# Performance work log

Measured on AMD Instinct MI355X. Metric: run time of the kernel, lower is better.

Reference implementation:

```python
import jax, jax.numpy as jnp
import numpy as np

D_MODEL = 1024  # scaling uses sqrt(d_model), as in the source


def setup_inputs() -> dict:
    key = jax.random.key(0)
    kx, kq, kk, kv = jax.random.split(key, 4)
    B, N, D, H = 4, 4096, D_MODEL, 128
    X = jax.random.normal(kx, (B, N, D), dtype=jnp.float32)
    # nn.Linear(d_model, d_head, bias=False) weights, stored as [d_model, d_head]
    s = 1.0 / np.sqrt(D)
    Wq = jax.random.normal(kq, (D, H), dtype=jnp.float32) * s
    Wk = jax.random.normal(kk, (D, H), dtype=jnp.float32) * s
    Wv = jax.random.normal(kv, (D, H), dtype=jnp.float32) * s
    return {"X": X, "Wq": Wq, "Wk": Wk, "Wv": Wv}


def reference(X, Wq, Wk, Wv):
    # Q, K, V: [B, N, H]
    Q = jnp.einsum("bnd,dh->bnh", X, Wq)
    K = jnp.einsum("bnd,dh->bnh", X, Wk)
    V = jnp.einsum("bnd,dh->bnh", X, Wv)
    # Scores: [B, N, N]; source divides by sqrt(d_model) (not sqrt(d_head))
    A = jnp.einsum("bqh,bkh->bqk", Q, K) / jnp.sqrt(jnp.float32(D_MODEL))
    A = jax.nn.softmax(A, axis=-1)
    # Dropout is identity in eval mode (deterministic reference baseline)
    return jnp.einsum("bqk,bkh->bqh", A, V)
```

## Files before the change

kernel.cpp:

```cpp
#include <hip/hip_runtime.h>
#include <stdint.h>

typedef __bf16 bf16_t;
typedef bf16_t bf16x8 __attribute__((ext_vector_type(8)));
typedef float f32x4 __attribute__((ext_vector_type(4)));
typedef float f32x16 __attribute__((ext_vector_type(16)));
typedef unsigned short u16;
typedef unsigned int u32;

#define MFMA16(a, b, c) __builtin_amdgcn_mfma_f32_16x16x32_bf16((a), (b), (c), 0, 0, 0)
#define MFMA32(a, b, c) __builtin_amdgcn_mfma_f32_32x32x16_bf16((a), (b), (c), 0, 0, 0)

#define QSCALE 0.04508422002778633f

__device__ __forceinline__ u16 f2bf(float f) {
  union { float f; unsigned u; } v; v.f = f;
  unsigned r = v.u + 0x7fffu + ((v.u >> 16) & 1u);
  return (u16)(r >> 16);
}

__device__ __forceinline__ float exp2x(float x) {
#if __has_builtin(__builtin_amdgcn_exp2f)
  return __builtin_amdgcn_exp2f(x);
#else
  return exp2f(x);
#endif
}

__device__ __forceinline__ float rcpx(float x) {
#if __has_builtin(__builtin_amdgcn_rcpf)
  return __builtin_amdgcn_rcpf(x);
#else
  return 1.0f / x;
#endif
}

__device__ __forceinline__ void async_cp16(const void* g, void* l) {
  __builtin_amdgcn_global_load_lds(
      (__attribute__((address_space(1))) void*)(void*)g,
      (__attribute__((address_space(3))) void*)l, 16, 0, 0);
}

__device__ __forceinline__ u32 cvtpk(float lo, float hi) {
  u32 r;
  asm("v_cvt_pk_bf16_f32 %0, %1, %2" : "=v"(r) : "v"(lo), "v"(hi));
  return r;
}
__device__ __forceinline__ void pl32swap(u32& a, u32& b) {
  asm volatile("v_permlane32_swap_b32 %0, %1" : "+v"(a), "+v"(b));
}

__global__ __launch_bounds__(256) void pack_w_k(const float* __restrict__ Wq,
                                                const float* __restrict__ Wk,
                                                const float* __restrict__ Wv,
                                                u16* __restrict__ wp) {
  int t = blockIdx.x * 256 + threadIdx.x;
  int mat = t >> 14;
  int rr = t & 16383;
  int frag = rr >> 6, lane = rr & 63;
  int nt = frag >> 5, kc = frag & 31;
  const float* W = (mat == 0) ? Wq : ((mat == 1) ? Wk : Wv);
  int k0 = kc * 32 + ((lane >> 4) << 3);
  int col = nt * 16 + (lane & 15);
  union { u16 h[8]; uint4 q; } u_;
#pragma unroll
  for (int j = 0; j < 8; ++j) u_.h[j] = f2bf(W[(size_t)(k0 + j) * 128 + col]);
  *(uint4*)(wp + (size_t)t * 8) = u_.q;
}

__global__ __launch_bounds__(256) void qkv_k(const float* __restrict__ X,
                                             const u16* __restrict__ wp,
                                             u16* __restrict__ Qb,
                                             u16* __restrict__ Kb,
                                             u16* __restrict__ Vt) {
  __shared__ __align__(16) char xs[2][4096];
  const int tid = threadIdx.x;
  const int w = tid >> 6, lane = tid & 63;
  const int r16 = lane >> 4, c16 = lane & 15;
  const int m0 = blockIdx.x * 32;

  f32x4 acc[2][6];
#pragma unroll
  for (int mt = 0; mt < 2; ++mt)
#pragma unroll
    for (int i = 0; i < 6; ++i) acc[mt][i] = (f32x4){0.f, 0.f, 0.f, 0.f};

  const int srow = tid >> 3, scol = tid & 7;
  const float* sbase = X + (size_t)(m0 + srow) * 1024 + scol * 8;
  const int soff = srow * 128 + ((scol * 16) ^ ((srow & 7) << 4));

  {
    float4 v0 = *(const float4*)(sbase);
    float4 v1 = *(const float4*)(sbase + 4);
    union { u16 h[8]; uint4 q; } u_;
    u_.h[0] = f2bf(v0.x); u_.h[1] = f2bf(v0.y); u_.h[2] = f2bf(v0.z); u_.h[3] = f2bf(v0.w);
    u_.h[4] = f2bf(v1.x); u_.h[5] = f2bf(v1.y); u_.h[6] = f2bf(v1.z); u_.h[7] = f2bf(v1.w);
    *(uint4*)(xs[0] + soff) = u_.q;
  }
  __syncthreads();

  for (int kc = 0; kc < 16; ++kc) {
    float4 n0, n1;
    const bool pfch = (kc + 1) < 16;
    if (pfch) {
      n0 = *(const float4*)(sbase + (kc + 1) * 64);
      n1 = *(const float4*)(sbase + (kc + 1) * 64 + 4);
    }
    const char* xb = xs[kc & 1];
    bf16x8 a[2][2];
#pragma unroll
    for (int mt = 0; mt < 2; ++mt)
#pragma unroll
      for (int ks = 0; ks < 2; ++ks) {
        int row = mt * 16 + c16;
        int off = row * 128 + (((ks * 64) + r16 * 16) ^ ((row & 7) << 4));
        a[mt][ks] = *(const bf16x8*)(xb + off);
      }
#pragma unroll
    for (int i = 0; i < 6; ++i) {
      int t = w + 4 * i;
      int mat = t >> 3, nt = t & 7;
      const u16* bp = wp + (size_t)mat * 131072 +
                      (size_t)((nt * 32 + kc * 2) * 64 + lane) * 8;
#pragma unroll
      for (int ks = 0; ks < 2; ++ks) {
        bf16x8 b = *(const bf16x8*)(bp + (size_t)ks * 512);
#pragma unroll
        for (int mt = 0; mt < 2; ++mt) acc[mt][i] = MFMA16(a[mt][ks], b, acc[mt][i]);
      }
    }
    if (pfch) {
      union { u16 h[8]; uint4 q; } u_;
      u_.h[0] = f2bf(n0.x); u_.h[1] = f2bf(n0.y); u_.h[2] = f2bf(n0.z); u_.h[3] = f2bf(n0.w);
      u_.h[4] = f2bf(n1.x); u_.h[5] = f2bf(n1.y); u_.h[6] = f2bf(n1.z); u_.h[7] = f2bf(n1.w);
      *(uint4*)(xs[(kc + 1) & 1] + soff) = u_.q;
    }
    __syncthreads();
  }

  const int batch = m0 >> 12;
#pragma unroll
  for (int i = 0; i < 6; ++i) {
    int t = w + 4 * i;
    int mat = t >> 3, nt = t & 7;
#pragma unroll
    for (int mt = 0; mt < 2; ++mt) {
      f32x4 v = acc[mt][i];
      if (mat == 2) {
        int d = nt * 16 + c16;
        int nloc = (m0 & 4095) + mt * 16 + r16 * 4;
        union { u16 h[4]; uint2 q; } u_;
#pragma unroll
        for (int r = 0; r < 4; ++r) u_.h[r] = f2bf(v[r]);
        *(uint2*)(Vt + ((size_t)(batch * 128 + d)) * 4096 + nloc) = u_.q;
      } else {
        u16* dstm = (mat == 0) ? Qb : Kb;
        float sc = (mat == 0) ? QSCALE : 1.0f;
#pragma unroll
        for (int r = 0; r < 4; ++r) {
          int row = m0 + mt * 16 + r16 * 4 + r;
          dstm[(size_t)row * 128 + nt * 16 + c16] = f2bf(v[r] * sc);
        }
      }
    }
  }
}

__global__ __launch_bounds__(256) void pack_kv_k(const u16* __restrict__ Kb,
                                                 const u16* __restrict__ Vt,
                                                 u16* __restrict__ Kf,
                                                 u16* __restrict__ Vf) {
  int t = blockIdx.x * 256 + threadIdx.x;
  int lane = t & 63, l31 = lane & 31, hi = (lane >> 5) & 1;
  if (t < 262144) {
    int frag = t >> 6;
    int batch = frag >> 10, kt = (frag >> 3) & 127, kc = frag & 7;
    const u16* src = Kb + ((size_t)batch * 4096 + kt * 32 + l31) * 128 + kc * 16 + hi * 8;
    *(uint4*)(Kf + (size_t)t * 8) = *(const uint4*)src;
  } else {
    int o = t - 262144;
    int frag = o >> 6;
    int batch = frag >> 10, tt = (frag >> 4) & 63, ks = (frag >> 2) & 3, dt = frag & 3;
    const u16* src = Vt + ((size_t)batch * 128 + dt * 32 + l31) * 4096 + tt * 64 + ks * 16 + hi * 8;
    *(uint4*)(Vf + (size_t)o * 8) = *(const uint4*)src;
  }
}

__device__ __forceinline__ void stage16(const char* src, char* dst, int tid) {
#pragma unroll
  for (int i = 0; i < 4; ++i)
    async_cp16(src + i * 4096 + tid * 16, dst + i * 4096 + tid * 16);
}

__global__ __launch_bounds__(256, 3) void attn_k(const u16* __restrict__ Qb,
                                                 const u16* __restrict__ Kf,
                                                 const u16* __restrict__ Vf,
                                                 _Float16* __restrict__ Opart,
                                                 float* __restrict__ Ml,
                                                 int nsplit) {
  __shared__ __align__(16) char smem[49152];
  const int tid = threadIdx.x;
  const int w = tid >> 6, lane = tid & 63;
  const int l31 = lane & 31, hi = lane >> 5;

  const int B = gridDim.x;
  int xcd = blockIdx.x & 7, idx = blockIdx.x >> 3;
  int linear = xcd * (B >> 3) + idx;
  int qt = linear & 31, g = linear >> 5;
  int batch = g / nsplit, split = g - batch * nsplit;
  const int q0 = qt * 128;
  const int t0 = (split * 64) / nsplit;
  const int t1 = ((split + 1) * 64) / nsplit;
  const int T = t1 - t0;

  const char* kfc = (const char*)Kf + (size_t)batch * 1048576 + (size_t)t0 * 16384;
  const char* vfc = (const char*)Vf + (size_t)batch * 1048576 + (size_t)t0 * 16384;

  bf16x8 qf[8];
  const u16* qrow = Qb + ((size_t)batch * 4096 + q0 + w * 32 + l31) * 128 + hi * 8;
#pragma unroll
  for (int kc = 0; kc < 8; ++kc) qf[kc] = *(const bf16x8*)(qrow + kc * 16);

  f32x16 acc[4];
#pragma unroll
  for (int dt = 0; dt < 4; ++dt)
#pragma unroll
    for (int j = 0; j < 16; ++j) acc[dt][j] = 0.f;
  float lacc[8];
#pragma unroll
  for (int i = 0; i < 8; ++i) lacc[i] = 0.f;

  char* vbuf = smem + 32768;
  stage16(vfc, vbuf, tid);
  stage16(kfc, smem, tid);
  if (T > 1) stage16(kfc + 16384, smem + 16384, tid);

  for (int t = 0; t < T; ++t) {
    if (t + 1 < T) {
      asm volatile("s_waitcnt vmcnt(4)" ::: "memory");
    } else {
      asm volatile("s_waitcnt vmcnt(0)" ::: "memory");
    }
    __builtin_amdgcn_s_barrier();
    asm volatile("" ::: "memory");
    const char* kb = smem + (t & 1) * 16384;

    f32x16 sv[2];
    __builtin_amdgcn_s_setprio(1);
#pragma unroll
    for (int nt = 0; nt < 2; ++nt) {
      f32x16 s = {};
#pragma unroll
      for (int kc = 0; kc < 8; ++kc) {
        bf16x8 kf = *(const bf16x8*)(kb + (nt * 8 + kc) * 1024 + lane * 16);
        s = MFMA32(kf, qf[kc], s);
      }
      sv[nt] = s;
    }
    __builtin_amdgcn_s_setprio(0);

#pragma unroll
    for (int nt = 0; nt < 2; ++nt)
#pragma unroll
      for (int i = 0; i < 16; ++i) sv[nt][i] = exp2x(sv[nt][i]);
#pragma unroll
    for (int i = 0; i < 8; ++i)
      lacc[i] += (sv[0][i] + sv[0][i + 8]) + (sv[1][i] + sv[1][i + 8]);

    bf16x8 pf[4];
#pragma unroll
    for (int nt = 0; nt < 2; ++nt)
#pragma unroll
      for (int half = 0; half < 2; ++half) {
        const float* p = (const float*)&sv[nt] + half * 8;
        u32 a0 = cvtpk(p[0], p[1]);
        u32 b0 = cvtpk(p[4], p[5]);
        u32 c0 = cvtpk(p[2], p[3]);
        u32 d0 = cvtpk(p[6], p[7]);
        pl32swap(a0, b0);
        pl32swap(c0, d0);
        union { u32 u[4]; bf16x8 v; } pu;
        pu.u[0] = a0; pu.u[1] = c0; pu.u[2] = b0; pu.u[3] = d0;
        pf[nt * 2 + half] = pu.v;
      }

    __builtin_amdgcn_s_setprio(1);
#pragma unroll
    for (int dt = 0; dt < 4; ++dt) {
#pragma unroll
      for (int ks = 0; ks < 4; ++ks) {
        bf16x8 vf = *(const bf16x8*)(vbuf + (ks * 4 + dt) * 1024 + lane * 16);
        acc[dt] = MFMA32(pf[ks], vf, acc[dt]);
      }
    }
    __builtin_amdgcn_s_setprio(0);

    asm volatile("" ::: "memory");
    __builtin_amdgcn_s_barrier();
    asm volatile("" ::: "memory");

    if (t + 1 < T) stage16(vfc + (size_t)(t + 1) * 16384, vbuf, tid);
    if (t + 2 < T) stage16(kfc + (size_t)(t + 2) * 16384, smem + (t & 1) * 16384, tid);
  }

  float ltot = ((lacc[0] + lacc[1]) + (lacc[2] + lacc[3])) +
               ((lacc[4] + lacc[5]) + (lacc[6] + lacc[7]));
  ltot += __shfl_xor(ltot, 32);

  size_t obase = (size_t)split * 16384 + (size_t)batch * 4096 + q0 + w * 32;
#pragma unroll
  for (int dt = 0; dt < 4; ++dt)
#pragma unroll
    for (int r = 0; r < 16; ++r) {
      int qr = (r & 3) + 8 * (r >> 2) + 4 * hi;
      float lq = __shfl(ltot, qr);
      Opart[(obase + qr) * 128 + dt * 32 + l31] = (_Float16)(acc[dt][r] * rcpx(lq));
    }
  if (lane < 32)
    Ml[(size_t)split * 16384 + (size_t)batch * 4096 + q0 + w * 32 + lane] = ltot;
}

template <int S>
__global__ __launch_bounds__(256) void reduce_k(const _Float16* __restrict__ Op,
                                                const float* __restrict__ Ml,
                                                float* __restrict__ Out) {
  int t = blockIdx.x * 256 + threadIdx.x;
  int q = t >> 4, d8 = (t & 15) << 3;
  float ls[S];
  float L = 0.f;
#pragma unroll
  for (int s = 0; s < S; ++s) {
    ls[s] = Ml[(size_t)s * 16384 + q];
    L += ls[s];
  }
  float o[8] = {0.f, 0.f, 0.f, 0.f, 0.f, 0.f, 0.f, 0.f};
#pragma unroll
  for (int s = 0; s < S; ++s) {
    union { uint4 u; _Float16 h[8]; } pv;
    pv.u = *(const uint4*)(Op + ((size_t)s * 16384 + q) * 128 + d8);
#pragma unroll
    for (int j = 0; j < 8; ++j) o[j] += (float)pv.h[j] * ls[s];
  }
  float inv = rcpx(L);
  float4 r0 = {o[0] * inv, o[1] * inv, o[2] * inv, o[3] * inv};
  float4 r1 = {o[4] * inv, o[5] * inv, o[6] * inv, o[7] * inv};
  *(float4*)(Out + (size_t)q * 128 + d8) = r0;
  *(float4*)(Out + (size_t)q * 128 + d8 + 4) = r1;
}

extern "C" void kernel_launch(void* const* d_in, const int* in_sizes, int n_in,
                              void* d_out, int out_size, void* d_ws, size_t ws_size,
                              hipStream_t stream) {
  const float* X  = (const float*)d_in[0];
  const float* Wq = (const float*)d_in[1];
  const float* Wk = (const float*)d_in[2];
  const float* Wv = (const float*)d_in[3];
  float* Out = (float*)d_out;
  char* ws = (char*)d_ws;
  u16* Qb = (u16*)(ws);
  u16* Kf = (u16*)(ws + (4u << 20));
  u16* Vf = (u16*)(ws + (8u << 20));
  _Float16* Opart = (_Float16*)(ws + (12u << 20));
  u16* Kb = (u16*)(ws + (12u << 20));
  u16* Vt = (u16*)(ws + (16u << 20));
  u16* Wp = (u16*)(ws + (20u << 20));

  int S = (ws_size >= (12ull << 20) + 6ull * (4194304ull + 65536ull)) ? 6 : 4;
  float* Ml = (float*)(ws + (12ull << 20) + (size_t)S * 4194304ull);

  pack_w_k<<<dim3(192), dim3(256), 0, stream>>>(Wq, Wk, Wv, Wp);
  qkv_k<<<dim3(512), dim3(256), 0, stream>>>(X, Wp, Qb, Kb, Vt);
  pack_kv_k<<<dim3(2048), dim3(256), 0, stream>>>(Kb, Vt, Kf, Vf);
  attn_k<<<dim3(128 * S), dim3(256), 0, stream>>>(Qb, Kf, Vf, Opart, Ml, S);
  if (S == 6)
    reduce_k<6><<<dim3(1024), dim3(256), 0, stream>>>(Opart, Ml, Out);
  else
    reduce_k<4><<<dim3(1024), dim3(256), 0, stream>>>(Opart, Ml, Out);
}
```

Measured before the change: 96.34 us.

## Drop K/V repack kernel and stage X asynchronously as fp32 in QKV projection

Measured after the change: 94.34 us. 2.1% less time.

```diff
diff --git a/kernel.cpp b/kernel.cpp
--- a/kernel.cpp
+++ b/kernel.cpp
@@ -68,16 +68,29 @@
   *(uint4*)(wp + (size_t)t * 8) = u_.q;
 }
 
+__device__ __forceinline__ void qkv_stage(const char* Xb, char* dst, int m0,
+                                          int kc, int tid) {
+#pragma unroll
+  for (int i = 0; i < 2; ++i) {
+    int p = i * 4096 + tid * 16;
+    int row = p >> 8, cb = p & 255;
+    int ucb = cb ^ ((row & 7) << 4);
+    async_cp16(Xb + ((size_t)(m0 + row) * 4096 + (size_t)kc * 256 + ucb),
+               dst + p);
+  }
+}
+
 __global__ __launch_bounds__(256) void qkv_k(const float* __restrict__ X,
                                              const u16* __restrict__ wp,
                                              u16* __restrict__ Qb,
                                              u16* __restrict__ Kb,
                                              u16* __restrict__ Vt) {
-  __shared__ __align__(16) char xs[2][4096];
+  __shared__ __align__(16) char xs[2][8192];
   const int tid = threadIdx.x;
   const int w = tid >> 6, lane = tid & 63;
   const int r16 = lane >> 4, c16 = lane & 15;
   const int m0 = blockIdx.x * 32;
+  const char* Xb = (const char*)X;
 
   f32x4 acc[2][6];
 #pragma unroll
@@ -85,57 +98,58 @@
 #pragma unroll
     for (int i = 0; i < 6; ++i) acc[mt][i] = (f32x4){0.f, 0.f, 0.f, 0.f};
 
-  const int srow = tid >> 3, scol = tid & 7;
-  const float* sbase = X + (size_t)(m0 + srow) * 1024 + scol * 8;
-  const int soff = srow * 128 + ((scol * 16) ^ ((srow & 7) << 4));
-
-  {
-    float4 v0 = *(const float4*)(sbase);
-    float4 v1 = *(const float4*)(sbase + 4);
-    union { u16 h[8]; uint4 q; } u_;
-    u_.h[0] = f2bf(v0.x); u_.h[1] = f2bf(v0.y); u_.h[2] = f2bf(v0.z); u_.h[3] = f2bf(v0.w);
-    u_.h[4] = f2bf(v1.x); u_.h[5] = f2bf(v1.y); u_.h[6] = f2bf(v1.z); u_.h[7] = f2bf(v1.w);
-    *(uint4*)(xs[0] + soff) = u_.q;
-  }
-  __syncthreads();
+  qkv_stage(Xb, xs[0], m0, 0, tid);
+  qkv_stage(Xb, xs[1], m0, 1, tid);
 
   for (int kc = 0; kc < 16; ++kc) {
-    float4 n0, n1;
-    const bool pfch = (kc + 1) < 16;
-    if (pfch) {
-      n0 = *(const float4*)(sbase + (kc + 1) * 64);
-      n1 = *(const float4*)(sbase + (kc + 1) * 64 + 4);
-    }
+    if (kc + 1 < 16) {
+      asm volatile("s_waitcnt vmcnt(2)" ::: "memory");
+    } else {
+      asm volatile("s_waitcnt vmcnt(0)" ::: "memory");
+    }
+    __builtin_amdgcn_s_barrier();
+    asm volatile("" ::: "memory");
+
     const char* xb = xs[kc & 1];
-    bf16x8 a[2][2];
-#pragma unroll
-    for (int mt = 0; mt < 2; ++mt)
-#pragma unroll
-      for (int ks = 0; ks < 2; ++ks) {
-        int row = mt * 16 + c16;
-        int off = row * 128 + (((ks * 64) + r16 * 16) ^ ((row & 7) << 4));
-        a[mt][ks] = *(const bf16x8*)(xb + off);
-      }
+    bf16x8 bw[6][2];
 #pragma unroll
     for (int i = 0; i < 6; ++i) {
       int t = w + 4 * i;
       int mat = t >> 3, nt = t & 7;
       const u16* bp = wp + (size_t)mat * 131072 +
                       (size_t)((nt * 32 + kc * 2) * 64 + lane) * 8;
+      bw[i][0] = *(const bf16x8*)(bp);
+      bw[i][1] = *(const bf16x8*)(bp + 512);
+    }
+    bf16x8 a[2][2];
+#pragma unroll
+    for (int mt = 0; mt < 2; ++mt)
 #pragma unroll
       for (int ks = 0; ks < 2; ++ks) {
-        bf16x8 b = *(const bf16x8*)(bp + (size_t)ks * 512);
-#pragma unroll
-        for (int mt = 0; mt < 2; ++mt) acc[mt][i] = MFMA16(a[mt][ks], b, acc[mt][i]);
-      }
-    }
-    if (pfch) {
-      union { u16 h[8]; uint4 q; } u_;
-      u_.h[0] = f2bf(n0.x); u_.h[1] = f2bf(n0.y); u_.h[2] = f2bf(n0.z); u_.h[3] = f2bf(n0.w);
-      u_.h[4] = f2bf(n1.x); u_.h[5] = f2bf(n1.y); u_.h[6] = f2bf(n1.z); u_.h[7] = f2bf(n1.w);
-      *(uint4*)(xs[(kc + 1) & 1] + soff) = u_.q;
-    }
-    __syncthreads();
+        int row = mt * 16 + c16;
+        int swz = (row & 7) << 4;
+        int cb0 = ks * 128 + r16 * 32;
+        f32x4 lo = *(const f32x4*)(xb + row * 256 + (cb0 ^ swz));
+        f32x4 hi = *(const f32x4*)(xb + row * 256 + ((cb0 + 16) ^ swz));
+        union { u32 u[4]; bf16x8 v; } pu;
+        pu.u[0] = cvtpk(lo[0], lo[1]);
+        pu.u[1] = cvtpk(lo[2], lo[3]);
+        pu.u[2] = cvtpk(hi[0], hi[1]);
+        pu.u[3] = cvtpk(hi[2], hi[3]);
+        a[mt][ks] = pu.v;
+      }
+#pragma unroll
+    for (int i = 0; i < 6; ++i)
+#pragma unroll
+      for (int ks = 0; ks < 2; ++ks)
+#pragma unroll
+        for (int mt = 0; mt < 2; ++mt)
+          acc[mt][i] = MFMA16(a[mt][ks], bw[i][ks], acc[mt][i]);
+
+    asm volatile("" ::: "memory");
+    __builtin_amdgcn_s_barrier();
+    asm volatile("" ::: "memory");
+    if (kc + 2 < 16) qkv_stage(Xb, xs[kc & 1], m0, kc + 2, tid);
   }
 
   const int batch = m0 >> 12;
@@ -166,35 +180,23 @@
   }
 }
 
-__global__ __launch_bounds__(256) void pack_kv_k(const u16* __restrict__ Kb,
+#define STAGE_K(t)                                                        \
+  {                                                                       \
+    const char* s_ = kbase + (size_t)(t) * 16384;                         \
+    char* d_ = smem + ((t) & 1) * 16384;                                  \
+    _Pragma("unroll") for (int i_ = 0; i_ < 4; ++i_)                      \
+        async_cp16(s_ + koff[i_], d_ + ldof[i_]);                         \
+  }
+#define STAGE_V(t)                                                        \
+  {                                                                       \
+    const char* s_ = vbase + (size_t)(t) * 128;                           \
+    _Pragma("unroll") for (int i_ = 0; i_ < 4; ++i_)                      \
+        async_cp16(s_ + voff[i_], vbuf + ldof[i_]);                       \
+  }
+
+__global__ __launch_bounds__(256, 3) void attn_k(const u16* __restrict__ Qb,
+                                                 const u16* __restrict__ Kb,
                                                  const u16* __restrict__ Vt,
-                                                 u16* __restrict__ Kf,
-                                                 u16* __restrict__ Vf) {
-  int t = blockIdx.x * 256 + threadIdx.x;
-  int lane = t & 63, l31 = lane & 31, hi = (lane >> 5) & 1;
-  if (t < 262144) {
-    int frag = t >> 6;
-    int batch = frag >> 10, kt = (frag >> 3) & 127, kc = frag & 7;
-    const u16* src = Kb + ((size_t)batch * 4096 + kt * 32 + l31) * 128 + kc * 16 + hi * 8;
-    *(uint4*)(Kf + (size_t)t * 8) = *(const uint4*)src;
-  } else {
-    int o = t - 262144;
-    int frag = o >> 6;
-    int batch = frag >> 10, tt = (frag >> 4) & 63, ks = (frag >> 2) & 3, dt = frag & 3;
-    const u16* src = Vt + ((size_t)batch * 128 + dt * 32 + l31) * 4096 + tt * 64 + ks * 16 + hi * 8;
-    *(uint4*)(Vf + (size_t)o * 8) = *(const uint4*)src;
-  }
-}
-
-__device__ __forceinline__ void stage16(const char* src, char* dst, int tid) {
-#pragma unroll
-  for (int i = 0; i < 4; ++i)
-    async_cp16(src + i * 4096 + tid * 16, dst + i * 4096 + tid * 16);
-}
-
-__global__ __launch_bounds__(256, 3) void attn_k(const u16* __restrict__ Qb,
-                                                 const u16* __restrict__ Kf,
-                                                 const u16* __restrict__ Vf,
                                                  _Float16* __restrict__ Opart,
                                                  float* __restrict__ Ml,
                                                  int nsplit) {
@@ -213,8 +215,21 @@
   const int t1 = ((split + 1) * 64) / nsplit;
   const int T = t1 - t0;
 
-  const char* kfc = (const char*)Kf + (size_t)batch * 1048576 + (size_t)t0 * 16384;
-  const char* vfc = (const char*)Vf + (size_t)batch * 1048576 + (size_t)t0 * 16384;
+  const char* kbase = (const char*)Kb + ((size_t)batch * 4096 + t0 * 64) * 256;
+  const char* vbase = (const char*)Vt +
+                      ((size_t)batch * 128 * 4096 + (size_t)t0 * 64) * 2;
+  char* vbuf = smem + 32768;
+
+  int koff[4], voff[4], ldof[4];
+#pragma unroll
+  for (int i = 0; i < 4; ++i) {
+    int frag = i * 4 + w;
+    int knt = frag >> 3, kkc = frag & 7;
+    koff[i] = ((knt * 32 + l31) * 128 + kkc * 16 + hi * 8) * 2;
+    int vks = frag >> 2, vdt = frag & 3;
+    voff[i] = ((vdt * 32 + l31) * 4096 + vks * 16 + hi * 8) * 2;
+    ldof[i] = i * 4096 + tid * 16;
+  }
 
   bf16x8 qf[8];
   const u16* qrow = Qb + ((size_t)batch * 4096 + q0 + w * 32 + l31) * 128 + hi * 8;
@@ -230,16 +245,15 @@
 #pragma unroll
   for (int i = 0; i < 8; ++i) lacc[i] = 0.f;
 
-  char* vbuf = smem + 32768;
-  stage16(vfc, vbuf, tid);
-  stage16(kfc, smem, tid);
-  if (T > 1) stage16(kfc + 16384, smem + 16384, tid);
+  STAGE_K(0);
+  STAGE_V(0);
+  if (T > 1) STAGE_K(1);
 
   for (int t = 0; t < T; ++t) {
     if (t + 1 < T) {
+      asm volatile("s_waitcnt vmcnt(8)" ::: "memory");
+    } else {
       asm volatile("s_waitcnt vmcnt(4)" ::: "memory");
-    } else {
-      asm volatile("s_waitcnt vmcnt(0)" ::: "memory");
     }
     __builtin_amdgcn_s_barrier();
     asm volatile("" ::: "memory");
@@ -284,6 +298,14 @@
         pf[nt * 2 + half] = pu.v;
       }
 
+    if (t + 1 < T) {
+      asm volatile("s_waitcnt vmcnt(4)" ::: "memory");
+    } else {
+      asm volatile("s_waitcnt vmcnt(0)" ::: "memory");
+    }
+    __builtin_amdgcn_s_barrier();
+    asm volatile("" ::: "memory");
+
     __builtin_amdgcn_s_setprio(1);
 #pragma unroll
     for (int dt = 0; dt < 4; ++dt) {
@@ -299,8 +321,8 @@
     __builtin_amdgcn_s_barrier();
     asm volatile("" ::: "memory");
 
-    if (t + 1 < T) stage16(vfc + (size_t)(t + 1) * 16384, vbuf, tid);
-    if (t + 2 < T) stage16(kfc + (size_t)(t + 2) * 16384, smem + (t & 1) * 16384, tid);
+    if (t + 1 < T) STAGE_V(t + 1);
+    if (t + 2 < T) STAGE_K(t + 2);
   }
 
   float ltot = ((lacc[0] + lacc[1]) + (lacc[2] + lacc[3])) +
@@ -358,20 +380,17 @@
   float* Out = (float*)d_out;
   char* ws = (char*)d_ws;
   u16* Qb = (u16*)(ws);
-  u16* Kf = (u16*)(ws + (4u << 20));
-  u16* Vf = (u16*)(ws + (8u << 20));
-  _Float16* Opart = (_Float16*)(ws + (12u << 20));
-  u16* Kb = (u16*)(ws + (12u << 20));
-  u16* Vt = (u16*)(ws + (16u << 20));
-  u16* Wp = (u16*)(ws + (20u << 20));
-
-  int S = (ws_size >= (12ull << 20) + 6ull * (4194304ull + 65536ull)) ? 6 : 4;
-  float* Ml = (float*)(ws + (12ull << 20) + (size_t)S * 4194304ull);
+  u16* Kb = (u16*)(ws + (4u << 20));
+  u16* Vt = (u16*)(ws + (8u << 20));
+  u16* Wp = (u16*)(ws + (12u << 20));
+  _Float16* Opart = (_Float16*)(ws + (13u << 20));
+
+  int S = (ws_size >= (13ull << 20) + 6ull * (4194304ull + 65536ull)) ? 6 : 4;
+  float* Ml = (float*)(ws + (13ull << 20) + (size_t)S * 4194304ull);
 
   pack_w_k<<<dim3(192), dim3(256), 0, stream>>>(Wq, Wk, Wv, Wp);
   qkv_k<<<dim3(512), dim3(256), 0, stream>>>(X, Wp, Qb, Kb, Vt);
-  pack_kv_k<<<dim3(2048), dim3(256), 0, stream>>>(Kb, Vt, Kf, Vf);
-  attn_k<<<dim3(128 * S), dim3(256), 0, stream>>>(Qb, Kf, Vf, Opart, Ml, S);
+  attn_k<<<dim3(128 * S), dim3(256), 0, stream>>>(Qb, Kb, Vt, Opart, Ml, S);
   if (S == 6)
     reduce_k<6><<<dim3(1024), dim3(256), 0, stream>>>(Opart, Ml, Out);
   else
```
